# Performance work log

Hardware: AMD Instinct MI355X
Metric: run time of the kernel (lower is better)

Reference implementation:

```python
import jax, jax.numpy as jnp
import numpy as np

B, N, D, H = 4, 2048, 256, 4
DH = D // H
LN_EPS = 1e-5


def setup_inputs() -> dict:
    key = jax.random.key(0)
    ks = jax.random.split(key, 8)
    x = jax.random.normal(ks[0], (B, N, D), dtype=jnp.float32)
    adj = jax.random.randint(ks[1], (N, N), 0, 2, dtype=jnp.int32)
    # parameters (PyTorch Linear stores W as [out, in]; we store [out,in] and apply x @ W.T)
    W = jax.random.normal(ks[2], (D, D), dtype=jnp.float32) * (1.0 / np.sqrt(D))
    a_src = jax.random.normal(ks[3], (H, DH), dtype=jnp.float32)
    a_dst = jax.random.normal(ks[4], (H, DH), dtype=jnp.float32)
    Wo = jax.random.normal(ks[5], (D, D), dtype=jnp.float32) * (1.0 / np.sqrt(D))
    bo = jnp.zeros((D,), dtype=jnp.float32)
    gamma = jnp.ones((D,), dtype=jnp.float32)
    beta = jnp.zeros((D,), dtype=jnp.float32)
    return {"x": x, "adj": adj, "W": W, "a_src": a_src, "a_dst": a_dst,
            "Wo": Wo, "bo": bo, "gamma": gamma, "beta": beta}


def _layer_norm(y, gamma, beta):
    mu = jnp.mean(y, axis=-1, keepdims=True)
    var = jnp.mean((y - mu) ** 2, axis=-1, keepdims=True)
    return (y - mu) * jax.lax.rsqrt(var + LN_EPS) * gamma + beta


def reference(x, adj, W, a_src, a_dst, Wo, bo, gamma, beta):
    # dropout in eval mode (identity)
    b, n, d = x.shape
    h = (x @ W.T).reshape(b, n, H, DH).transpose(0, 2, 1, 3)  # [B,H,N,DH]
    src = jnp.einsum('bhnd,hd->bhn', h, a_src)  # [B,H,N]
    dst = jnp.einsum('bhnd,hd->bhn', h, a_dst)  # [B,H,N]
    e = src[:, :, :, None] + dst[:, :, None, :]  # e[b,h,i,j] = src_i + dst_j
    e = jnp.where(e >= 0, e, 0.2 * e)  # leaky_relu(0.2)
    mask = (adj > 0)[None, None, :, :]
    e = jnp.where(mask, e, -jnp.inf)
    attn = jax.nn.softmax(e, axis=-1)  # [B,H,N,N]
    out = jnp.einsum('bhij,bhjd->bhid', attn, h)  # [B,H,N,DH]
    out = out.transpose(0, 2, 1, 3).reshape(b, n, d)
    out = out @ Wo.T + bo
    return _layer_norm(x + out, gamma, beta)
```

## Files before the change

kernel.cpp:

```cpp
#include <hip/hip_runtime.h>
#include <stdint.h>

#define NTOK 2048
#define DMODEL 256
#define NHEAD 4

typedef __attribute__((ext_vector_type(8))) short short8;
typedef __attribute__((ext_vector_type(4))) float f32x4;

#define MFMA16(a, b, c) __builtin_amdgcn_mfma_f32_16x16x32_bf16(a, b, c, 0, 0, 0)

#if __has_builtin(__builtin_amdgcn_exp2f)
#define EXP2(x) __builtin_amdgcn_exp2f(x)
#else
#define EXP2(x) __expf((x) * 0.6931471805599453f)
#endif

__device__ __forceinline__ unsigned short f2bf(float f) {
  union { float f; unsigned int u; } v; v.f = f;
  unsigned int r = v.u + 0x7FFFu + ((v.u >> 16) & 1u);
  return (unsigned short)(r >> 16);
}

__device__ __forceinline__ f32x4 zero4() {
  f32x4 v; v[0] = 0.f; v[1] = 0.f; v[2] = 0.f; v[3] = 0.f; return v;
}

__global__ void k_prep_pack(const float* __restrict__ x, const float* __restrict__ W,
                            const float* __restrict__ Wo, const int* __restrict__ adj,
                            unsigned short* __restrict__ xbf, unsigned short* __restrict__ Wbf,
                            unsigned short* __restrict__ Wobf,
                            unsigned long long* __restrict__ bits) {
  const int b = blockIdx.x;
  if (b < 2176) {
    int e = (b * 256 + threadIdx.x) * 4;
    const float* s; unsigned short* d; int off;
    if (e < 2097152)              { s = x;  d = xbf;  off = e; }
    else if (e < 2097152 + 65536) { s = W;  d = Wbf;  off = e - 2097152; }
    else                          { s = Wo; d = Wobf; off = e - 2162688; }
    float4 v = *(const float4*)(s + off);
    ushort4 o;
    o.x = f2bf(v.x); o.y = f2bf(v.y); o.z = f2bf(v.z); o.w = f2bf(v.w);
    *(ushort4*)(d + off) = o;
  } else {
    int g = (b - 2176) * 256 + threadIdx.x;
    int v = adj[g];
    unsigned long long m = __ballot(v > 0);
    if ((threadIdx.x & 63) == 0) bits[g >> 6] = m;
  }
}

__global__ void k_gemm1(const unsigned short* __restrict__ xbf, const unsigned short* __restrict__ Wbf,
                        const float* __restrict__ a_src, const float* __restrict__ a_dst,
                        unsigned short* __restrict__ hT, float* __restrict__ srcv,
                        float* __restrict__ dstv) {
  __shared__ float tile[64][65];
  __shared__ float reds[2][4][64];
  const int tid = threadIdx.x, lane = tid & 63, w = tid >> 6;
  const int g0 = blockIdx.x * 64;
  const int hh = blockIdx.y;
  const int n0 = hh * 64;
  const int l15 = lane & 15, kl = (lane >> 4) * 8;

  const unsigned short* arow = xbf + (size_t)(g0 + w * 16 + l15) * 256 + kl;
  const unsigned short* brow = Wbf + (size_t)(n0 + l15) * 256 + kl;

  f32x4 acc[4];
#pragma unroll
  for (int nf = 0; nf < 4; ++nf) acc[nf] = zero4();

#pragma unroll
  for (int k = 0; k < 256; k += 32) {
    short8 a = *(const short8*)(arow + k);
#pragma unroll
    for (int nf = 0; nf < 4; ++nf) {
      short8 b = *(const short8*)(brow + nf * 4096 + k);
      acc[nf] = MFMA16(a, b, acc[nf]);
    }
  }

  const int rbase = w * 16 + (lane >> 4) * 4;
#pragma unroll
  for (int nf = 0; nf < 4; ++nf)
#pragma unroll
    for (int r = 0; r < 4; ++r)
      tile[rbase + r][nf * 16 + l15] = acc[nf][r];
  __syncthreads();

  const int bh = (g0 >> 11) * NHEAD + hh;
  {
    const int dh = tid >> 2, nq = (tid & 3) * 16;
    unsigned short* dp = hT + ((size_t)bh * 64 + dh) * 2048 + (g0 & 2047) + nq;
    short8 v0, v1;
#pragma unroll
    for (int q = 0; q < 8; ++q) v0[q] = (short)f2bf(tile[nq + q][dh]);
#pragma unroll
    for (int q = 0; q < 8; ++q) v1[q] = (short)f2bf(tile[nq + 8 + q][dh]);
    *(short8*)dp = v0;
    *(short8*)(dp + 8) = v1;
  }
  {
    const int n_loc = tid & 63, q4 = tid >> 6;
    const float* as = a_src + hh * 64 + q4 * 16;
    const float* ad = a_dst + hh * 64 + q4 * 16;
    float ps = 0.f, pd = 0.f;
#pragma unroll
    for (int d2 = 0; d2 < 16; ++d2) {
      float hv = tile[n_loc][q4 * 16 + d2];
      ps += hv * as[d2];
      pd += hv * ad[d2];
    }
    reds[0][q4][n_loc] = ps;
    reds[1][q4][n_loc] = pd;
  }
  __syncthreads();
  if (tid < 64) {
    float s = reds[0][0][tid] + reds[0][1][tid] + reds[0][2][tid] + reds[0][3][tid];
    float d = reds[1][0][tid] + reds[1][1][tid] + reds[1][2][tid] + reds[1][3][tid];
    srcv[(size_t)bh * 2048 + (g0 & 2047) + tid] = s;
    dstv[(size_t)bh * 2048 + (g0 & 2047) + tid] = d;
  }
}

__global__ __launch_bounds__(256) void k_attn(
    const unsigned short* __restrict__ hT, const float* __restrict__ srcv,
    const float* __restrict__ dstv, const unsigned long long* __restrict__ bits,
    unsigned short* __restrict__ attb) {
  __shared__ float dst_s[2048];
  __shared__ unsigned long long adjw[64][33];
  __shared__ float src_s[64];
  __shared__ float red[4];
  __shared__ unsigned short kv[2][8192];

  const int tid = threadIdx.x, lane = tid & 63, w = tid >> 6;
  const int orig = blockIdx.x;
  const int lid = (orig & 7) * 64 + (orig >> 3);
  const int bh = lid >> 5;
  const int i0 = (lid & 31) * 64;
  const float LOG2E = 1.4426950408889634f;

  float lmax = -3.0e38f;
  {
    const float* dsrc = dstv + (size_t)bh * 2048;
#pragma unroll
    for (int t = 0; t < 2; ++t) {
      int idx = (tid + t * 256) * 4;
      float4 v = *(const float4*)(dsrc + idx);
      v.x *= LOG2E; v.y *= LOG2E; v.z *= LOG2E; v.w *= LOG2E;
      *(float4*)(dst_s + idx) = v;
      lmax = fmaxf(fmaxf(fmaxf(lmax, v.x), fmaxf(v.y, v.z)), v.w);
    }
#pragma unroll
    for (int off = 32; off >= 1; off >>= 1) lmax = fmaxf(lmax, __shfl_xor(lmax, off));
    if (lane == 0) red[w] = lmax;
    if (tid < 64) src_s[tid] = srcv[(size_t)bh * 2048 + i0 + tid] * LOG2E;
#pragma unroll
    for (int t = 0; t < 8; ++t) {
      int q = tid + t * 256;
      adjw[q >> 5][q & 31] = bits[(size_t)(i0 + (q >> 5)) * 32 + (q & 31)];
    }
  }

  const unsigned short* hTb = hT + (size_t)bh * 131072;
  short8 st0, st1, st2, st3;
  const int c0 = tid, c1 = 256 + tid, c2 = 512 + tid, c3 = 768 + tid;
  const int dh0 = c0 >> 4, ci0 = c0 & 15;
  const int dh1 = c1 >> 4, ci1 = c1 & 15;
  const int dh2 = c2 >> 4, ci2 = c2 & 15;
  const int dh3 = c3 >> 4, ci3 = c3 & 15;
  const int wof0 = dh0 * 128 + ((ci0 ^ (dh0 & 7)) << 3);
  const int wof1 = dh1 * 128 + ((ci1 ^ (dh1 & 7)) << 3);
  const int wof2 = dh2 * 128 + ((ci2 ^ (dh2 & 7)) << 3);
  const int wof3 = dh3 * 128 + ((ci3 ^ (dh3 & 7)) << 3);
  st0 = *(const short8*)(hTb + dh0 * 2048 + ci0 * 8);
  st1 = *(const short8*)(hTb + dh1 * 2048 + ci1 * 8);
  st2 = *(const short8*)(hTb + dh2 * 2048 + ci2 * 8);
  st3 = *(const short8*)(hTb + dh3 * 2048 + ci3 * 8);
  *(short8*)(&kv[0][wof0]) = st0;
  *(short8*)(&kv[0][wof1]) = st1;
  *(short8*)(&kv[0][wof2]) = st2;
  *(short8*)(&kv[0][wof3]) = st3;
  __syncthreads();
  const float dmax = fmaxf(fmaxf(red[0], red[1]), fmaxf(red[2], red[3]));

  const int l15 = lane & 15, klg = lane >> 4, kl = klg * 8;
  const int il = w * 16 + l15;
  const float src_i = src_s[il];
  const float sm0 = src_i + dmax;
  const float m = fmaxf(sm0, 0.2f * sm0);
  const int xm = l15 & 7;

  short8 ones;
#pragma unroll
  for (int q = 0; q < 8; ++q) ones[q] = (short)0x3F80;

  float lv = m; (void)lv;
  f32x4 acc[4], accs;
#pragma unroll
  for (int nf = 0; nf < 4; ++nf) acc[nf] = zero4();
  accs = zero4();

  for (int t = 0; t < 16; ++t) {
    const int cur = t & 1;
    if (t < 15) {
      const unsigned short* src = hTb + (t + 1) * 128;
      st0 = *(const short8*)(src + dh0 * 2048 + ci0 * 8);
      st1 = *(const short8*)(src + dh1 * 2048 + ci1 * 8);
      st2 = *(const short8*)(src + dh2 * 2048 + ci2 * 8);
      st3 = *(const short8*)(src + dh3 * 2048 + ci3 * 8);
    }
    const unsigned long long w0 = adjw[il][2 * t], w1 = adjw[il][2 * t + 1];
    const unsigned short* kvb = kv[cur];
    const float* dsb = dst_s + t * 128;
#pragma unroll
    for (int jj = 0; jj < 4; ++jj) {
      float4 d0 = *(const float4*)(dsb + jj * 32 + kl);
      float4 d1 = *(const float4*)(dsb + jj * 32 + kl + 4);
      const unsigned int byte =
          (unsigned int)(((jj < 2 ? w0 : w1) >> ((jj & 1) * 32 + kl))) & 0xFFu;
      float dv[8] = {d0.x, d0.y, d0.z, d0.w, d1.x, d1.y, d1.z, d1.w};
      float p[8];
#pragma unroll
      for (int t8 = 0; t8 < 8; ++t8) {
        float e = src_i + dv[t8];
        e = fmaxf(e, 0.2f * e);
        float s = ((byte >> t8) & 1u) ? (e - m) : -3.0e38f;
        p[t8] = EXP2(s);
      }
      union { short8 s8; unsigned int u32[4]; } af;
#pragma unroll
      for (int q = 0; q < 4; ++q)
        asm("v_cvt_pk_bf16_f32 %0, %1, %2" : "=v"(af.u32[q]) : "v"(p[2 * q]), "v"(p[2 * q + 1]));
      const int chunk = (((jj * 4 + klg) ^ xm) << 3) + l15 * 128;
      accs = MFMA16(af.s8, ones, accs);
#pragma unroll
      for (int nf = 0; nf < 4; ++nf) {
        short8 bfrag = *(const short8*)(kvb + nf * 2048 + chunk);
        acc[nf] = MFMA16(af.s8, bfrag, acc[nf]);
      }
    }
    __syncthreads();
    if (t < 15) {
      unsigned short* kvn = kv[cur ^ 1];
      *(short8*)(&kvn[wof0]) = st0;
      *(short8*)(&kvn[wof1]) = st1;
      *(short8*)(&kvn[wof2]) = st2;
      *(short8*)(&kvn[wof3]) = st3;
    }
    __syncthreads();
  }

  const int rb = klg * 4;
  float linv[4];
#pragma unroll
  for (int r = 0; r < 4; ++r) linv[r] = 1.f / accs[r];
  const int b = bh >> 2, hh2 = bh & 3;
#pragma unroll
  for (int nf = 0; nf < 4; ++nf)
#pragma unroll
    for (int r = 0; r < 4; ++r) {
      int i = i0 + w * 16 + rb + r;
      size_t o = ((size_t)(b * 2048 + i)) * 256 + hh2 * 64 + nf * 16 + l15;
      attb[o] = f2bf(acc[nf][r] * linv[r]);
    }
}

__global__ void k_gemm2(const unsigned short* __restrict__ attb, const unsigned short* __restrict__ Wobf,
                        const float* __restrict__ bo, const float* __restrict__ x,
                        const float* __restrict__ gamma, const float* __restrict__ beta,
                        float* __restrict__ out) {
  __shared__ float tile[32][260];
  const int tid = threadIdx.x, lane = tid & 63, w = tid >> 6;
  const int g0 = blockIdx.x * 32;
  const int l15 = lane & 15, kl = (lane >> 4) * 8;
  const int rw = (w & 1) * 16;
  const int cb = (w >> 1) * 128;

  const unsigned short* arow = attb + (size_t)(g0 + rw + l15) * 256 + kl;
  const unsigned short* brow = Wobf + (size_t)(cb + l15) * 256 + kl;

  f32x4 acc[8];
#pragma unroll
  for (int nf = 0; nf < 8; ++nf) acc[nf] = zero4();

#pragma unroll
  for (int k = 0; k < 256; k += 32) {
    short8 a = *(const short8*)(arow + k);
#pragma unroll
    for (int nf = 0; nf < 8; ++nf) {
      short8 b = *(const short8*)(brow + (size_t)nf * 4096 + k);
      acc[nf] = MFMA16(a, b, acc[nf]);
    }
  }

  const int rb = rw + (lane >> 4) * 4;
#pragma unroll
  for (int nf = 0; nf < 8; ++nf)
#pragma unroll
    for (int r = 0; r < 4; ++r) {
      int c = cb + nf * 16 + l15;
      tile[rb + r][c] = acc[nf][r] + bo[c];
    }
  __syncthreads();

  const float4 gv = *(const float4*)(gamma + lane * 4);
  const float4 bv = *(const float4*)(beta + lane * 4);
  for (int r = 0; r < 8; ++r) {
    const int gl = w * 8 + r;
    const size_t g = g0 + gl;
    float4 xv = *(const float4*)(x + g * 256 + lane * 4);
    float4 tv = *(float4*)(&tile[gl][lane * 4]);
    float v0 = tv.x + xv.x, v1 = tv.y + xv.y, v2 = tv.z + xv.z, v3 = tv.w + xv.w;
    float sum = v0 + v1 + v2 + v3;
    float sq = v0 * v0 + v1 * v1 + v2 * v2 + v3 * v3;
#pragma unroll
    for (int off = 32; off >= 1; off >>= 1) {
      sum += __shfl_xor(sum, off);
      sq += __shfl_xor(sq, off);
    }
    const float mu = sum * (1.f / 256.f);
    const float var = sq * (1.f / 256.f) - mu * mu;
    const float rs = rsqrtf(var + 1e-5f);
    float4 o;
    o.x = (v0 - mu) * rs * gv.x + bv.x;
    o.y = (v1 - mu) * rs * gv.y + bv.y;
    o.z = (v2 - mu) * rs * gv.z + bv.z;
    o.w = (v3 - mu) * rs * gv.w + bv.w;
    *(float4*)(out + g * 256 + lane * 4) = o;
  }
}

extern "C" void kernel_launch(void* const* d_in, const int* in_sizes, int n_in,
                              void* d_out, int out_size, void* d_ws, size_t ws_size,
                              hipStream_t stream) {
  const float* x      = (const float*)d_in[0];
  const int*   adj    = (const int*)d_in[1];
  const float* W      = (const float*)d_in[2];
  const float* a_src  = (const float*)d_in[3];
  const float* a_dst  = (const float*)d_in[4];
  const float* Wo     = (const float*)d_in[5];
  const float* bo     = (const float*)d_in[6];
  const float* gamma  = (const float*)d_in[7];
  const float* beta   = (const float*)d_in[8];
  float* out = (float*)d_out;

  char* ws = (char*)d_ws;
  unsigned short* xbf       = (unsigned short*)(ws);
  unsigned short* hT        = (unsigned short*)(ws + (4u << 20));
  unsigned short* attb      = (unsigned short*)(ws + (8u << 20));
  unsigned long long* bits  = (unsigned long long*)(ws + (12u << 20));
  unsigned short* Wbf       = (unsigned short*)(ws + (12u << 20) + (512u << 10));
  unsigned short* Wobf      = (unsigned short*)(ws + (12u << 20) + (640u << 10));
  float* srcv               = (float*)(ws + (12u << 20) + (768u << 10));
  float* dstv               = (float*)(ws + (12u << 20) + (896u << 10));

  k_prep_pack<<<18560, 256, 0, stream>>>(x, W, Wo, adj, xbf, Wbf, Wobf, bits);
  k_gemm1<<<dim3(128, 4), 256, 0, stream>>>(xbf, Wbf, a_src, a_dst, hT, srcv, dstv);
  k_attn<<<512, 256, 0, stream>>>(hT, srcv, dstv, bits, attb);
  k_gemm2<<<256, 256, 0, stream>>>(attb, Wobf, bo, x, gamma, beta, out);
}
```

Baseline: 69.53 us.

## Split attention key loop across eight waves with cross-wave reduction

The attention kernel now runs 512 threads per block. Waves are arranged as 2 row-groups × 4 key-slices: each wave handles 32 query rows over one quarter of every key tile, reusing each loaded B fragment for two row halves. Partial accumulators and row sums are combined through shared memory in a serial three-step reduction before the final normalisation and store. One of the two barriers per tile iteration is also dropped. This trades extra LDS reduction traffic, barriers and higher register pressure (launch bounds 512,4) for more waves per block and a shorter per-wave inner loop.

```diff
diff --git a/kernel.cpp b/kernel.cpp
--- a/kernel.cpp
+++ b/kernel.cpp
@@ -122,83 +122,80 @@
   }
 }
 
-__global__ __launch_bounds__(256) void k_attn(
+__global__ __launch_bounds__(512, 4) void k_attn(
     const unsigned short* __restrict__ hT, const float* __restrict__ srcv,
     const float* __restrict__ dstv, const unsigned long long* __restrict__ bits,
     unsigned short* __restrict__ attb) {
   __shared__ float dst_s[2048];
   __shared__ unsigned long long adjw[64][33];
   __shared__ float src_s[64];
-  __shared__ float red[4];
+  __shared__ float red[8];
   __shared__ unsigned short kv[2][8192];
+  __shared__ float comb[2][64][40];
 
   const int tid = threadIdx.x, lane = tid & 63, w = tid >> 6;
   const int orig = blockIdx.x;
   const int lid = (orig & 7) * 64 + (orig >> 3);
   const int bh = lid >> 5;
   const int i0 = (lid & 31) * 64;
+  const int rg = w & 1, js = w >> 1;
   const float LOG2E = 1.4426950408889634f;
 
   float lmax = -3.0e38f;
   {
     const float* dsrc = dstv + (size_t)bh * 2048;
-#pragma unroll
-    for (int t = 0; t < 2; ++t) {
-      int idx = (tid + t * 256) * 4;
-      float4 v = *(const float4*)(dsrc + idx);
-      v.x *= LOG2E; v.y *= LOG2E; v.z *= LOG2E; v.w *= LOG2E;
-      *(float4*)(dst_s + idx) = v;
-      lmax = fmaxf(fmaxf(fmaxf(lmax, v.x), fmaxf(v.y, v.z)), v.w);
-    }
+    int idx = tid * 4;
+    float4 v = *(const float4*)(dsrc + idx);
+    v.x *= LOG2E; v.y *= LOG2E; v.z *= LOG2E; v.w *= LOG2E;
+    *(float4*)(dst_s + idx) = v;
+    lmax = fmaxf(fmaxf(v.x, v.y), fmaxf(v.z, v.w));
 #pragma unroll
     for (int off = 32; off >= 1; off >>= 1) lmax = fmaxf(lmax, __shfl_xor(lmax, off));
     if (lane == 0) red[w] = lmax;
     if (tid < 64) src_s[tid] = srcv[(size_t)bh * 2048 + i0 + tid] * LOG2E;
 #pragma unroll
-    for (int t = 0; t < 8; ++t) {
-      int q = tid + t * 256;
+    for (int t = 0; t < 4; ++t) {
+      int q = tid + t * 512;
       adjw[q >> 5][q & 31] = bits[(size_t)(i0 + (q >> 5)) * 32 + (q & 31)];
     }
   }
 
   const unsigned short* hTb = hT + (size_t)bh * 131072;
-  short8 st0, st1, st2, st3;
-  const int c0 = tid, c1 = 256 + tid, c2 = 512 + tid, c3 = 768 + tid;
+  const int c0 = tid, c1 = tid + 512;
   const int dh0 = c0 >> 4, ci0 = c0 & 15;
   const int dh1 = c1 >> 4, ci1 = c1 & 15;
-  const int dh2 = c2 >> 4, ci2 = c2 & 15;
-  const int dh3 = c3 >> 4, ci3 = c3 & 15;
   const int wof0 = dh0 * 128 + ((ci0 ^ (dh0 & 7)) << 3);
   const int wof1 = dh1 * 128 + ((ci1 ^ (dh1 & 7)) << 3);
-  const int wof2 = dh2 * 128 + ((ci2 ^ (dh2 & 7)) << 3);
-  const int wof3 = dh3 * 128 + ((ci3 ^ (dh3 & 7)) << 3);
-  st0 = *(const short8*)(hTb + dh0 * 2048 + ci0 * 8);
-  st1 = *(const short8*)(hTb + dh1 * 2048 + ci1 * 8);
-  st2 = *(const short8*)(hTb + dh2 * 2048 + ci2 * 8);
-  st3 = *(const short8*)(hTb + dh3 * 2048 + ci3 * 8);
+  short8 st0 = *(const short8*)(hTb + dh0 * 2048 + ci0 * 8);
+  short8 st1 = *(const short8*)(hTb + dh1 * 2048 + ci1 * 8);
   *(short8*)(&kv[0][wof0]) = st0;
   *(short8*)(&kv[0][wof1]) = st1;
-  *(short8*)(&kv[0][wof2]) = st2;
-  *(short8*)(&kv[0][wof3]) = st3;
   __syncthreads();
-  const float dmax = fmaxf(fmaxf(red[0], red[1]), fmaxf(red[2], red[3]));
+  const float dmax = fmaxf(fmaxf(fmaxf(red[0], red[1]), fmaxf(red[2], red[3])),
+                           fmaxf(fmaxf(red[4], red[5]), fmaxf(red[6], red[7])));
 
   const int l15 = lane & 15, klg = lane >> 4, kl = klg * 8;
-  const int il = w * 16 + l15;
-  const float src_i = src_s[il];
-  const float sm0 = src_i + dmax;
-  const float m = fmaxf(sm0, 0.2f * sm0);
+  const float src0 = src_s[rg * 32 + l15];
+  const float src1 = src_s[rg * 32 + 16 + l15];
+  const float sa0 = src0 + dmax, sa1 = src1 + dmax;
+  const float m0 = fmaxf(sa0, 0.2f * sa0);
+  const float m1 = fmaxf(sa1, 0.2f * sa1);
   const int xm = l15 & 7;
+  const int chunk = (((js * 4 + klg) ^ xm) << 3) + l15 * 128;
+  const int il0 = rg * 32 + l15, il1 = il0 + 16;
+  const int wsel = js >> 1, wsh = (js & 1) * 32 + kl;
 
   short8 ones;
 #pragma unroll
   for (int q = 0; q < 8; ++q) ones[q] = (short)0x3F80;
 
-  float lv = m; (void)lv;
-  f32x4 acc[4], accs;
-#pragma unroll
-  for (int nf = 0; nf < 4; ++nf) acc[nf] = zero4();
-  accs = zero4();
+  f32x4 acc[2][4], accs[2];
+#pragma unroll
+  for (int rh = 0; rh < 2; ++rh) {
+    accs[rh] = zero4();
+#pragma unroll
+    for (int nf = 0; nf < 4; ++nf) acc[rh][nf] = zero4();
+  }
 
   for (int t = 0; t < 16; ++t) {
     const int cur = t & 1;
@@ -206,19 +203,21 @@
       const unsigned short* src = hTb + (t + 1) * 128;
       st0 = *(const short8*)(src + dh0 * 2048 + ci0 * 8);
       st1 = *(const short8*)(src + dh1 * 2048 + ci1 * 8);
-      st2 = *(const short8*)(src + dh2 * 2048 + ci2 * 8);
-      st3 = *(const short8*)(src + dh3 * 2048 + ci3 * 8);
-    }
-    const unsigned long long w0 = adjw[il][2 * t], w1 = adjw[il][2 * t + 1];
+    }
     const unsigned short* kvb = kv[cur];
-    const float* dsb = dst_s + t * 128;
-#pragma unroll
-    for (int jj = 0; jj < 4; ++jj) {
-      float4 d0 = *(const float4*)(dsb + jj * 32 + kl);
-      float4 d1 = *(const float4*)(dsb + jj * 32 + kl + 4);
-      const unsigned int byte =
-          (unsigned int)(((jj < 2 ? w0 : w1) >> ((jj & 1) * 32 + kl))) & 0xFFu;
-      float dv[8] = {d0.x, d0.y, d0.z, d0.w, d1.x, d1.y, d1.z, d1.w};
+    short8 bf[4];
+#pragma unroll
+    for (int nf = 0; nf < 4; ++nf) bf[nf] = *(const short8*)(kvb + nf * 2048 + chunk);
+    const float* dsb = dst_s + t * 128 + js * 32;
+    float4 d0 = *(const float4*)(dsb + kl);
+    float4 d1 = *(const float4*)(dsb + kl + 4);
+    float dv[8] = {d0.x, d0.y, d0.z, d0.w, d1.x, d1.y, d1.z, d1.w};
+#pragma unroll
+    for (int rh = 0; rh < 2; ++rh) {
+      const float src_i = rh ? src1 : src0;
+      const float m = rh ? m1 : m0;
+      const unsigned long long word = adjw[rh ? il1 : il0][2 * t + wsel];
+      const unsigned int byte = (unsigned int)(word >> wsh) & 0xFFu;
       float p[8];
 #pragma unroll
       for (int t8 = 0; t8 < 8; ++t8) {
@@ -231,38 +230,64 @@
 #pragma unroll
       for (int q = 0; q < 4; ++q)
         asm("v_cvt_pk_bf16_f32 %0, %1, %2" : "=v"(af.u32[q]) : "v"(p[2 * q]), "v"(p[2 * q + 1]));
-      const int chunk = (((jj * 4 + klg) ^ xm) << 3) + l15 * 128;
-      accs = MFMA16(af.s8, ones, accs);
-#pragma unroll
-      for (int nf = 0; nf < 4; ++nf) {
-        short8 bfrag = *(const short8*)(kvb + nf * 2048 + chunk);
-        acc[nf] = MFMA16(af.s8, bfrag, acc[nf]);
-      }
-    }
-    __syncthreads();
+      accs[rh] = MFMA16(af.s8, ones, accs[rh]);
+#pragma unroll
+      for (int nf = 0; nf < 4; ++nf) acc[rh][nf] = MFMA16(af.s8, bf[nf], acc[rh][nf]);
+    }
     if (t < 15) {
       unsigned short* kvn = kv[cur ^ 1];
       *(short8*)(&kvn[wof0]) = st0;
       *(short8*)(&kvn[wof1]) = st1;
-      *(short8*)(&kvn[wof2]) = st2;
-      *(short8*)(&kvn[wof3]) = st3;
     }
     __syncthreads();
   }
 
-  const int rb = klg * 4;
-  float linv[4];
-#pragma unroll
-  for (int r = 0; r < 4; ++r) linv[r] = 1.f / accs[r];
-  const int b = bh >> 2, hh2 = bh & 3;
-#pragma unroll
-  for (int nf = 0; nf < 4; ++nf)
-#pragma unroll
-    for (int r = 0; r < 4; ++r) {
-      int i = i0 + w * 16 + rb + r;
-      size_t o = ((size_t)(b * 2048 + i)) * 256 + hh2 * 64 + nf * 16 + l15;
-      attb[o] = f2bf(acc[nf][r] * linv[r]);
-    }
+#pragma unroll 1
+  for (int s = 1; s < 4; ++s) {
+    if (js == s) {
+#pragma unroll
+      for (int rh = 0; rh < 2; ++rh) {
+#pragma unroll
+        for (int nf = 0; nf < 4; ++nf)
+#pragma unroll
+          for (int r = 0; r < 4; ++r) comb[rg][lane][rh * 20 + nf * 4 + r] = acc[rh][nf][r];
+#pragma unroll
+        for (int r = 0; r < 4; ++r) comb[rg][lane][rh * 20 + 16 + r] = accs[rh][r];
+      }
+    }
+    __syncthreads();
+    if (js == 0) {
+#pragma unroll
+      for (int rh = 0; rh < 2; ++rh) {
+#pragma unroll
+        for (int nf = 0; nf < 4; ++nf)
+#pragma unroll
+          for (int r = 0; r < 4; ++r) acc[rh][nf][r] += comb[rg][lane][rh * 20 + nf * 4 + r];
+#pragma unroll
+        for (int r = 0; r < 4; ++r) accs[rh][r] += comb[rg][lane][rh * 20 + 16 + r];
+      }
+    }
+    __syncthreads();
+  }
+
+  if (js == 0) {
+    const int rb = klg * 4;
+    const int b = bh >> 2, hh2 = bh & 3;
+#pragma unroll
+    for (int rh = 0; rh < 2; ++rh) {
+      float linv[4];
+#pragma unroll
+      for (int r = 0; r < 4; ++r) linv[r] = 1.f / accs[rh][r];
+#pragma unroll
+      for (int nf = 0; nf < 4; ++nf)
+#pragma unroll
+        for (int r = 0; r < 4; ++r) {
+          int i = i0 + rg * 32 + rh * 16 + rb + r;
+          size_t o = ((size_t)(b * 2048 + i)) * 256 + hh2 * 64 + nf * 16 + l15;
+          attb[o] = f2bf(acc[rh][nf][r] * linv[r]);
+        }
+    }
+  }
 }
 
 __global__ void k_gemm2(const unsigned short* __restrict__ attb, const unsigned short* __restrict__ Wobf,
@@ -356,6 +381,6 @@
 
   k_prep_pack<<<18560, 256, 0, stream>>>(x, W, Wo, adj, xbf, Wbf, Wobf, bits);
   k_gemm1<<<dim3(128, 4), 256, 0, stream>>>(xbf, Wbf, a_src, a_dst, hT, srcv, dstv);
-  k_attn<<<512, 256, 0, stream>>>(hT, srcv, dstv, bits, attb);
+  k_attn<<<512, 512, 0, stream>>>(hT, srcv, dstv, bits, attb);
   k_gemm2<<<256, 256, 0, stream>>>(attb, Wobf, bo, x, gamma, beta, out);
 }
```

After: 65.49 us. -5.8%, faster.
